# Kernel optimization log

Hardware: AMD Instinct MI355X
Metric: run time of the kernel (lower is better)

Reference implementation:

```python
import jax, jax.numpy as jnp
import numpy as np

# init_kwargs (closed over, matching BaseDepthVolumeModel.__init__)
DEPTH_START = 0.5
DEPTH_END = 10.0
DEPTH_NUM = 64

N_SAMPLES, N_VIEWS, HEIGHT, WIDTH = 2, 4, 256, 320


def _make_extrinsics(key, shape):
    """Random small-rotation-about-y + translation world->camera 4x4 matrices."""
    ang = jax.random.uniform(key, shape, minval=-0.2, maxval=0.2)
    c, s = jnp.cos(ang), jnp.sin(ang)
    z, o = jnp.zeros_like(ang), jnp.ones_like(ang)
    R = jnp.stack([c, z, s, z, o, z, -s, z, c], axis=-1).reshape(*shape, 3, 3)
    t = jax.random.uniform(jax.random.fold_in(key, 1), (*shape, 3), minval=-0.5, maxval=0.5)
    E = jnp.zeros((*shape, 4, 4), jnp.float32)
    E = E.at[..., :3, :3].set(R).at[..., :3, 3].set(t).at[..., 3, 3].set(1.0)
    return E.astype(jnp.float32)


def setup_inputs() -> dict:
    key = jax.random.key(0)
    k1, k2 = jax.random.split(key)
    fx = fy = 200.0
    K = jnp.array([[fx, 0.0, WIDTH / 2.0], [0.0, fy, HEIGHT / 2.0], [0.0, 0.0, 1.0]], jnp.float32)
    return {
        "dst_intrinsics": jnp.broadcast_to(K, (N_SAMPLES, 1, 3, 3)),
        "dst_extrinsics": _make_extrinsics(k1, (N_SAMPLES, 1)),
        "src_intrinsics": jnp.broadcast_to(K, (N_SAMPLES, N_VIEWS, 3, 3)),
        "src_extrinsics": _make_extrinsics(k2, (N_SAMPLES, N_VIEWS)),
        "n_samples": N_SAMPLES,
        "n_views": N_VIEWS,
        "height": HEIGHT,
        "width": WIDTH,
    }


def reference(dst_intrinsics, dst_extrinsics, src_intrinsics, src_extrinsics,
              n_samples, n_views, height, width):
    # Plane-sweep target->source projection for every (sample, view, depth, pixel),
    # fully batched instead of the original triple Python loop.
    depths = jnp.linspace(DEPTH_START, DEPTH_END, DEPTH_NUM).astype(jnp.float32)  # [D]

    Kd = dst_intrinsics[:, 0]                       # [N,3,3]
    Ed = dst_extrinsics[:, 0]                       # [N,4,4]
    # relative transform source_cam <- target_cam:  T = E_src @ inv(E_dst)
    T = jnp.einsum('nvij,njk->nvik', src_extrinsics, jnp.linalg.inv(Ed))  # [N,V,4,4]
    R, t = T[..., :3, :3], T[..., :3, 3]
    A = jnp.einsum('nvij,nvjk->nvik', src_intrinsics, R)                  # K_src @ R  [N,V,3,3]
    b = jnp.einsum('nvij,nvj->nvi', src_intrinsics, t)                    # K_src @ t  [N,V,3]

    # homogeneous pixel grid of the target view, [H,W,3]
    xs = jnp.arange(width, dtype=jnp.float32)
    ys = jnp.arange(height, dtype=jnp.float32)
    X, Y = jnp.meshgrid(xs, ys, indexing='xy')
    grid_h = jnp.stack([X, Y, jnp.ones_like(X)], axis=-1)                 # [H,W,3]

    rays = jnp.einsum('nij,hwj->nhwi', jnp.linalg.inv(Kd), grid_h)        # K_dst^-1 p  [N,H,W,3]
    base = jnp.einsum('nvij,nhwj->nvhwi', A, rays)                        # [N,V,H,W,3]
    # proj = d * (K_src R K_dst^-1 p) + K_src t  -> [N,V,D,H,W,3]
    proj = depths[None, None, :, None, None, None] * base[:, :, None] + b[:, :, None, None, None, :]

    z = proj[..., 2:3]
    z_safe = jnp.where(jnp.abs(z) < 1e-8, 1e-8, z)
    xy = proj[..., :2] / z_safe                                           # source pixel coords

    in_x = (xy[..., 0:1] >= 0.0) & (xy[..., 0:1] <= width - 1)
    in_y = (xy[..., 1:2] >= 0.0) & (xy[..., 1:2] <= height - 1)
    mask = (in_x & in_y & (z > 0.0)).astype(jnp.float32)                  # [N,V,D,H,W,1]

    return xy, mask
```

## Files before the change

kernel.cpp:

```cpp
#include <hip/hip_runtime.h>
#include <math.h>

#define N_S 2
#define N_V 4
#define DQ  64
#define HH  256
#define WW  320
#define WW2 (WW / 2)
#define DPT 16
#define NDC (DQ / DPT)

typedef float f32x4 __attribute__((ext_vector_type(4)));
typedef float f32x2 __attribute__((ext_vector_type(2)));

__global__ __launch_bounds__(256) void fused_warp_kernel(
    const float* __restrict__ Kd,
    const float* __restrict__ Ed,
    const float* __restrict__ Ks,
    const float* __restrict__ Es,
    float* __restrict__ out)
{
    const int HW = HH * WW;
    int idx = blockIdx.x * 256 + threadIdx.x;

    int w2 = idx % WW2;
    int tt = idx / WW2;
    int h  = tt % HH;
    tt /= HH;
    int dc = tt % NDC;
    int nv = tt / NDC;
    int n  = nv >> 2;

    const float* E = Ed + n * 16;
    float Ri[3][3], ti[3];
    #pragma unroll
    for (int r = 0; r < 3; ++r)
        #pragma unroll
        for (int c = 0; c < 3; ++c)
            Ri[r][c] = E[c * 4 + r];
    #pragma unroll
    for (int r = 0; r < 3; ++r)
        ti[r] = -(Ri[r][0] * E[3] + Ri[r][1] * E[7] + Ri[r][2] * E[11]);

    const float* S = Es + nv * 16;
    float Tr[3][3], Tt[3];
    #pragma unroll
    for (int r = 0; r < 3; ++r) {
        #pragma unroll
        for (int c = 0; c < 3; ++c)
            Tr[r][c] = S[r*4+0]*Ri[0][c] + S[r*4+1]*Ri[1][c] + S[r*4+2]*Ri[2][c];
        Tt[r] = S[r*4+0]*ti[0] + S[r*4+1]*ti[1] + S[r*4+2]*ti[2] + S[r*4+3];
    }

    const float* Kv = Ks + nv * 9;
    float A00,A01,A02,A10,A11,A12,A20,A21,A22,b0,b1,b2;
    {
        float Am[3][3], bm[3];
        #pragma unroll
        for (int r = 0; r < 3; ++r) {
            #pragma unroll
            for (int c = 0; c < 3; ++c)
                Am[r][c] = Kv[r*3+0]*Tr[0][c] + Kv[r*3+1]*Tr[1][c] + Kv[r*3+2]*Tr[2][c];
            bm[r] = Kv[r*3+0]*Tt[0] + Kv[r*3+1]*Tt[1] + Kv[r*3+2]*Tt[2];
        }
        A00=Am[0][0];A01=Am[0][1];A02=Am[0][2];
        A10=Am[1][0];A11=Am[1][1];A12=Am[1][2];
        A20=Am[2][0];A21=Am[2][1];A22=Am[2][2];
        b0=bm[0];b1=bm[1];b2=bm[2];
    }

    float ik0,ik1,ik2,ik3,ik4,ik5,ik6,ik7,ik8;
    {
        const float* Km = Kd + n * 9;
        float a=Km[0],b=Km[1],c=Km[2],d=Km[3],e=Km[4],f=Km[5],g=Km[6],hh=Km[7],k=Km[8];
        float det = a*(e*k - f*hh) - b*(d*k - f*g) + c*(d*hh - e*g);
        float inv = 1.0f / det;
        ik0 =  (e*k - f*hh) * inv;
        ik1 = -(b*k - c*hh) * inv;
        ik2 =  (b*f - c*e) * inv;
        ik3 = -(d*k - f*g) * inv;
        ik4 =  (a*k - c*g) * inv;
        ik5 = -(a*f - c*d) * inv;
        ik6 =  (d*hh - e*g) * inv;
        ik7 = -(a*hh - b*g) * inv;
        ik8 =  (a*e - b*d) * inv;
    }

    float X0 = (float)(2 * w2), X1 = X0 + 1.0f, Y = (float)h;

    float rx0 = ik0*X0 + ik1*Y + ik2;
    float ry0 = ik3*X0 + ik4*Y + ik5;
    float rz0 = ik6*X0 + ik7*Y + ik8;
    float rx1 = ik0*X1 + ik1*Y + ik2;
    float ry1 = ik3*X1 + ik4*Y + ik5;
    float rz1 = ik6*X1 + ik7*Y + ik8;

    float bx0 = A00*rx0 + A01*ry0 + A02*rz0;
    float by0 = A10*rx0 + A11*ry0 + A12*rz0;
    float bz0 = A20*rx0 + A21*ry0 + A22*rz0;
    float bx1 = A00*rx1 + A01*ry1 + A02*rz1;
    float by1 = A10*rx1 + A11*ry1 + A12*rz1;
    float bz1 = A20*rx1 + A21*ry1 + A22*rz1;

    size_t pixbase = ((size_t)nv * DQ + (size_t)dc * DPT) * HW
                   + (size_t)h * WW + (size_t)(2 * w2);
    float* __restrict__ mout = out + (size_t)N_S * N_V * DQ * HW * 2;

    const float step = (float)(9.5 / 63.0);
    int d0 = dc * DPT;

    #pragma unroll
    for (int j = 0; j < DPT; ++j) {
        float depth = 0.5f + (float)(d0 + j) * step;

        float px0 = depth*bx0 + b0, py0 = depth*by0 + b1, pz0 = depth*bz0 + b2;
        float px1 = depth*bx1 + b0, py1 = depth*by1 + b1, pz1 = depth*bz1 + b2;

        float zs0 = (fabsf(pz0) < 1e-8f) ? 1e-8f : pz0;
        float zs1 = (fabsf(pz1) < 1e-8f) ? 1e-8f : pz1;

        float x0 = px0 / zs0, y0 = py0 / zs0;
        float x1 = px1 / zs1, y1 = py1 / zs1;

        float m0 = (x0 >= 0.0f && x0 <= (float)(WW-1) &&
                    y0 >= 0.0f && y0 <= (float)(HH-1) && pz0 > 0.0f) ? 1.0f : 0.0f;
        float m1 = (x1 >= 0.0f && x1 <= (float)(WW-1) &&
                    y1 >= 0.0f && y1 <= (float)(HH-1) && pz1 > 0.0f) ? 1.0f : 0.0f;

        size_t p = pixbase + (size_t)j * HW;

        f32x4 xyv; xyv.x = x0; xyv.y = y0; xyv.z = x1; xyv.w = y1;
        __builtin_nontemporal_store(xyv, (f32x4*)(out + 2 * p));
        f32x2 mv; mv.x = m0; mv.y = m1;
        __builtin_nontemporal_store(mv, (f32x2*)(mout + p));
    }
}

extern "C" void kernel_launch(void* const* d_in, const int* in_sizes, int n_in,
                              void* d_out, int out_size, void* d_ws, size_t ws_size,
                              hipStream_t stream) {
    const float* Kd = (const float*)d_in[0];
    const float* Ed = (const float*)d_in[1];
    const float* Ks = (const float*)d_in[2];
    const float* Es = (const float*)d_in[3];

    const long long total = (long long)N_S * N_V * NDC * HH * WW2;
    int blocks = (int)((total + 255) / 256);
    hipLaunchKernelGGL(fused_warp_kernel, dim3(blocks), dim3(256), 0, stream,
                       Kd, Ed, Ks, Es, (float*)d_out);
}
```

Before: 94.95 us.

## Process four pixels per thread with wider stores and reciprocal-based division

Each thread now handles four adjacent pixels and eight depths instead of two pixels and sixteen depths. The mask can then be written with one 16-byte store and the coordinates with two, and an approximate hardware reciprocal with one Newton step replaces the two IEEE divisions per pixel. Launch bounds gain a minimum-occupancy hint. The reciprocal can differ from exact division in the last bits, which may flip mask values right at the image borders.

```diff
diff --git a/kernel.cpp b/kernel.cpp
--- a/kernel.cpp
+++ b/kernel.cpp
@@ -6,14 +6,14 @@
 #define DQ  64
 #define HH  256
 #define WW  320
-#define WW2 (WW / 2)
-#define DPT 16
+#define PX  4
+#define WW4 (WW / PX)
+#define DPT 8
 #define NDC (DQ / DPT)
 
 typedef float f32x4 __attribute__((ext_vector_type(4)));
-typedef float f32x2 __attribute__((ext_vector_type(2)));
 
-__global__ __launch_bounds__(256) void fused_warp_kernel(
+__global__ __launch_bounds__(256, 4) void fused_warp_kernel(
     const float* __restrict__ Kd,
     const float* __restrict__ Ed,
     const float* __restrict__ Ks,
@@ -23,8 +23,8 @@
     const int HW = HH * WW;
     int idx = blockIdx.x * 256 + threadIdx.x;
 
-    int w2 = idx % WW2;
-    int tt = idx / WW2;
+    int w4 = idx % WW4;
+    int tt = idx / WW4;
     int h  = tt % HH;
     tt /= HH;
     int dc = tt % NDC;
@@ -86,24 +86,21 @@
         ik8 =  (a*e - b*d) * inv;
     }
 
-    float X0 = (float)(2 * w2), X1 = X0 + 1.0f, Y = (float)h;
-
-    float rx0 = ik0*X0 + ik1*Y + ik2;
-    float ry0 = ik3*X0 + ik4*Y + ik5;
-    float rz0 = ik6*X0 + ik7*Y + ik8;
-    float rx1 = ik0*X1 + ik1*Y + ik2;
-    float ry1 = ik3*X1 + ik4*Y + ik5;
-    float rz1 = ik6*X1 + ik7*Y + ik8;
-
-    float bx0 = A00*rx0 + A01*ry0 + A02*rz0;
-    float by0 = A10*rx0 + A11*ry0 + A12*rz0;
-    float bz0 = A20*rx0 + A21*ry0 + A22*rz0;
-    float bx1 = A00*rx1 + A01*ry1 + A02*rz1;
-    float by1 = A10*rx1 + A11*ry1 + A12*rz1;
-    float bz1 = A20*rx1 + A21*ry1 + A22*rz1;
+    float Y = (float)h;
+    float bx[PX], by[PX], bz[PX];
+    #pragma unroll
+    for (int p = 0; p < PX; ++p) {
+        float X = (float)(PX * w4 + p);
+        float rx = ik0*X + ik1*Y + ik2;
+        float ry = ik3*X + ik4*Y + ik5;
+        float rz = ik6*X + ik7*Y + ik8;
+        bx[p] = A00*rx + A01*ry + A02*rz;
+        by[p] = A10*rx + A11*ry + A12*rz;
+        bz[p] = A20*rx + A21*ry + A22*rz;
+    }
 
     size_t pixbase = ((size_t)nv * DQ + (size_t)dc * DPT) * HW
-                   + (size_t)h * WW + (size_t)(2 * w2);
+                   + (size_t)h * WW + (size_t)(PX * w4);
     float* __restrict__ mout = out + (size_t)N_S * N_V * DQ * HW * 2;
 
     const float step = (float)(9.5 / 63.0);
@@ -113,26 +110,31 @@
     for (int j = 0; j < DPT; ++j) {
         float depth = 0.5f + (float)(d0 + j) * step;
 
-        float px0 = depth*bx0 + b0, py0 = depth*by0 + b1, pz0 = depth*bz0 + b2;
-        float px1 = depth*bx1 + b0, py1 = depth*by1 + b1, pz1 = depth*bz1 + b2;
+        float x[PX], y[PX], m[PX];
+        #pragma unroll
+        for (int p = 0; p < PX; ++p) {
+            float px = depth*bx[p] + b0;
+            float py = depth*by[p] + b1;
+            float pz = depth*bz[p] + b2;
+            float zs = (fabsf(pz) < 1e-8f) ? 1e-8f : pz;
+            float r  = __builtin_amdgcn_rcpf(zs);
+            r = r * (2.0f - zs * r);
+            x[p] = px * r;
+            y[p] = py * r;
+            m[p] = (x[p] >= 0.0f && x[p] <= (float)(WW-1) &&
+                    y[p] >= 0.0f && y[p] <= (float)(HH-1) &&
+                    pz > 0.0f) ? 1.0f : 0.0f;
+        }
 
-        float zs0 = (fabsf(pz0) < 1e-8f) ? 1e-8f : pz0;
-        float zs1 = (fabsf(pz1) < 1e-8f) ? 1e-8f : pz1;
+        size_t pp = pixbase + (size_t)j * HW;
 
-        float x0 = px0 / zs0, y0 = py0 / zs0;
-        float x1 = px1 / zs1, y1 = py1 / zs1;
+        f32x4 xy0; xy0.x = x[0]; xy0.y = y[0]; xy0.z = x[1]; xy0.w = y[1];
+        f32x4 xy1; xy1.x = x[2]; xy1.y = y[2]; xy1.z = x[3]; xy1.w = y[3];
+        f32x4 mv;  mv.x  = m[0]; mv.y  = m[1]; mv.z  = m[2]; mv.w  = m[3];
 
-        float m0 = (x0 >= 0.0f && x0 <= (float)(WW-1) &&
-                    y0 >= 0.0f && y0 <= (float)(HH-1) && pz0 > 0.0f) ? 1.0f : 0.0f;
-        float m1 = (x1 >= 0.0f && x1 <= (float)(WW-1) &&
-                    y1 >= 0.0f && y1 <= (float)(HH-1) && pz1 > 0.0f) ? 1.0f : 0.0f;
-
-        size_t p = pixbase + (size_t)j * HW;
-
-        f32x4 xyv; xyv.x = x0; xyv.y = y0; xyv.z = x1; xyv.w = y1;
-        __builtin_nontemporal_store(xyv, (f32x4*)(out + 2 * p));
-        f32x2 mv; mv.x = m0; mv.y = m1;
-        __builtin_nontemporal_store(mv, (f32x2*)(mout + p));
+        __builtin_nontemporal_store(xy0, (f32x4*)(out + 2 * pp));
+        __builtin_nontemporal_store(xy1, (f32x4*)(out + 2 * pp + 4));
+        __builtin_nontemporal_store(mv,  (f32x4*)(mout + pp));
     }
 }
 
@@ -144,7 +146,7 @@
     const float* Ks = (const float*)d_in[2];
     const float* Es = (const float*)d_in[3];
 
-    const long long total = (long long)N_S * N_V * NDC * HH * WW2;
+    const long long total = (long long)N_S * N_V * NDC * HH * WW4;
     int blocks = (int)((total + 255) / 256);
     hipLaunchKernelGGL(fused_warp_kernel, dim3(blocks), dim3(256), 0, stream,
                        Kd, Ed, Ks, Es, (float*)d_out);
```

Result: slower. 208.2 us (+119.3%).

## Restructure into per-depth-slice blocks with folded projection matrix and fast reciprocal

Applied to the files above, without the earlier changes.

Each block now handles one (view, depth) slice chunk and folds depth, K_src·R and K_dst^-1 into a single 3x3 affine map, so each pixel needs only a few FMAs. Blocks loop over contiguous pixels, so consecutive iterations write contiguous addresses within one slice instead of striding across depth planes. The per-pixel division is replaced by a hardware reciprocal plus one Newton step. This cuts per-pixel arithmetic but changes rounding relative to the reference's multiply-then-divide order, and it adds integer division by the width inside the loop.

```diff
diff --git a/kernel.cpp b/kernel.cpp
--- a/kernel.cpp
+++ b/kernel.cpp
@@ -6,30 +6,26 @@
 #define DQ  64
 #define HH  256
 #define WW  320
-#define WW2 (WW / 2)
-#define DPT 16
-#define NDC (DQ / DPT)
+#define HW  (HH * WW)
+#define SPLIT 8
+#define CHUNK_PX (HW / SPLIT)
+#define ITERS (CHUNK_PX / (256 * 2))
 
 typedef float f32x4 __attribute__((ext_vector_type(4)));
 typedef float f32x2 __attribute__((ext_vector_type(2)));
 
-__global__ __launch_bounds__(256) void fused_warp_kernel(
+__global__ __launch_bounds__(256) void slice_kernel(
     const float* __restrict__ Kd,
     const float* __restrict__ Ed,
     const float* __restrict__ Ks,
     const float* __restrict__ Es,
     float* __restrict__ out)
 {
-    const int HW = HH * WW;
-    int idx = blockIdx.x * 256 + threadIdx.x;
-
-    int w2 = idx % WW2;
-    int tt = idx / WW2;
-    int h  = tt % HH;
-    tt /= HH;
-    int dc = tt % NDC;
-    int nv = tt / NDC;
-    int n  = nv >> 2;
+    int bid   = blockIdx.x;
+    int chunk = bid % SPLIT;
+    int d     = (bid / SPLIT) % DQ;
+    int nv    = bid / (SPLIT * DQ);
+    int n     = nv >> 2;
 
     const float* E = Ed + n * 16;
     float Ri[3][3], ti[3];
@@ -53,86 +49,88 @@
     }
 
     const float* Kv = Ks + nv * 9;
-    float A00,A01,A02,A10,A11,A12,A20,A21,A22,b0,b1,b2;
-    {
-        float Am[3][3], bm[3];
+    float Am[3][3], bm[3];
+    #pragma unroll
+    for (int r = 0; r < 3; ++r) {
         #pragma unroll
-        for (int r = 0; r < 3; ++r) {
-            #pragma unroll
-            for (int c = 0; c < 3; ++c)
-                Am[r][c] = Kv[r*3+0]*Tr[0][c] + Kv[r*3+1]*Tr[1][c] + Kv[r*3+2]*Tr[2][c];
-            bm[r] = Kv[r*3+0]*Tt[0] + Kv[r*3+1]*Tt[1] + Kv[r*3+2]*Tt[2];
-        }
-        A00=Am[0][0];A01=Am[0][1];A02=Am[0][2];
-        A10=Am[1][0];A11=Am[1][1];A12=Am[1][2];
-        A20=Am[2][0];A21=Am[2][1];A22=Am[2][2];
-        b0=bm[0];b1=bm[1];b2=bm[2];
+        for (int c = 0; c < 3; ++c)
+            Am[r][c] = Kv[r*3+0]*Tr[0][c] + Kv[r*3+1]*Tr[1][c] + Kv[r*3+2]*Tr[2][c];
+        bm[r] = Kv[r*3+0]*Tt[0] + Kv[r*3+1]*Tt[1] + Kv[r*3+2]*Tt[2];
     }
 
-    float ik0,ik1,ik2,ik3,ik4,ik5,ik6,ik7,ik8;
+    float IK[3][3];
     {
         const float* Km = Kd + n * 9;
-        float a=Km[0],b=Km[1],c=Km[2],d=Km[3],e=Km[4],f=Km[5],g=Km[6],hh=Km[7],k=Km[8];
-        float det = a*(e*k - f*hh) - b*(d*k - f*g) + c*(d*hh - e*g);
+        float a=Km[0],b=Km[1],c=Km[2],dd=Km[3],e=Km[4],f=Km[5],g=Km[6],hh=Km[7],k=Km[8];
+        float det = a*(e*k - f*hh) - b*(dd*k - f*g) + c*(dd*hh - e*g);
         float inv = 1.0f / det;
-        ik0 =  (e*k - f*hh) * inv;
-        ik1 = -(b*k - c*hh) * inv;
-        ik2 =  (b*f - c*e) * inv;
-        ik3 = -(d*k - f*g) * inv;
-        ik4 =  (a*k - c*g) * inv;
-        ik5 = -(a*f - c*d) * inv;
-        ik6 =  (d*hh - e*g) * inv;
-        ik7 = -(a*hh - b*g) * inv;
-        ik8 =  (a*e - b*d) * inv;
+        IK[0][0] =  (e*k - f*hh) * inv;
+        IK[0][1] = -(b*k - c*hh) * inv;
+        IK[0][2] =  (b*f - c*e) * inv;
+        IK[1][0] = -(dd*k - f*g) * inv;
+        IK[1][1] =  (a*k - c*g) * inv;
+        IK[1][2] = -(a*f - c*dd) * inv;
+        IK[2][0] =  (dd*hh - e*g) * inv;
+        IK[2][1] = -(a*hh - b*g) * inv;
+        IK[2][2] =  (a*e - b*dd) * inv;
     }
 
-    float X0 = (float)(2 * w2), X1 = X0 + 1.0f, Y = (float)h;
+    const float step = (float)(9.5 / 63.0);
+    float depth = 0.5f + (float)d * step;
+    float Q[3][3], cvec[3];
+    #pragma unroll
+    for (int r = 0; r < 3; ++r) {
+        #pragma unroll
+        for (int c = 0; c < 3; ++c)
+            Q[r][c] = depth * (Am[r][0]*IK[0][c] + Am[r][1]*IK[1][c] + Am[r][2]*IK[2][c]);
+        cvec[r] = Q[r][2] + bm[r];
+    }
+    float Q00=Q[0][0], Q01=Q[0][1], c0=cvec[0];
+    float Q10=Q[1][0], Q11=Q[1][1], c1=cvec[1];
+    float Q20=Q[2][0], Q21=Q[2][1], c2=cvec[2];
 
-    float rx0 = ik0*X0 + ik1*Y + ik2;
-    float ry0 = ik3*X0 + ik4*Y + ik5;
-    float rz0 = ik6*X0 + ik7*Y + ik8;
-    float rx1 = ik0*X1 + ik1*Y + ik2;
-    float ry1 = ik3*X1 + ik4*Y + ik5;
-    float rz1 = ik6*X1 + ik7*Y + ik8;
+    size_t slice = (size_t)nv * DQ + (size_t)d;
+    float* __restrict__ xyp = out + slice * (size_t)HW * 2 + (size_t)chunk * CHUNK_PX * 2;
+    float* __restrict__ mp  = out + (size_t)N_S * N_V * DQ * HW * 2
+                            + slice * (size_t)HW + (size_t)chunk * CHUNK_PX;
 
-    float bx0 = A00*rx0 + A01*ry0 + A02*rz0;
-    float by0 = A10*rx0 + A11*ry0 + A12*rz0;
-    float bz0 = A20*rx0 + A21*ry0 + A22*rz0;
-    float bx1 = A00*rx1 + A01*ry1 + A02*rz1;
-    float by1 = A10*rx1 + A11*ry1 + A12*rz1;
-    float bz1 = A20*rx1 + A21*ry1 + A22*rz1;
+    int t2 = threadIdx.x * 2;
+    int gbase = chunk * CHUNK_PX + t2;
 
-    size_t pixbase = ((size_t)nv * DQ + (size_t)dc * DPT) * HW
-                   + (size_t)h * WW + (size_t)(2 * w2);
-    float* __restrict__ mout = out + (size_t)N_S * N_V * DQ * HW * 2;
+    #pragma unroll 4
+    for (int j = 0; j < ITERS; ++j) {
+        int pix  = j * 512 + t2;
+        int gpix = gbase + j * 512;
+        int h = gpix / WW;
+        int w = gpix - h * WW;
+        float X = (float)w, Y = (float)h;
 
-    const float step = (float)(9.5 / 63.0);
-    int d0 = dc * DPT;
-
-    #pragma unroll
-    for (int j = 0; j < DPT; ++j) {
-        float depth = 0.5f + (float)(d0 + j) * step;
-
-        float px0 = depth*bx0 + b0, py0 = depth*by0 + b1, pz0 = depth*bz0 + b2;
-        float px1 = depth*bx1 + b0, py1 = depth*by1 + b1, pz1 = depth*bz1 + b2;
+        float px0 = Q00*X + Q01*Y + c0;
+        float py0 = Q10*X + Q11*Y + c1;
+        float pz0 = Q20*X + Q21*Y + c2;
+        float px1 = px0 + Q00;
+        float py1 = py0 + Q10;
+        float pz1 = pz0 + Q20;
 
         float zs0 = (fabsf(pz0) < 1e-8f) ? 1e-8f : pz0;
         float zs1 = (fabsf(pz1) < 1e-8f) ? 1e-8f : pz1;
+        float r0 = __builtin_amdgcn_rcpf(zs0);
+        r0 = r0 * (2.0f - zs0 * r0);
+        float r1 = __builtin_amdgcn_rcpf(zs1);
+        r1 = r1 * (2.0f - zs1 * r1);
 
-        float x0 = px0 / zs0, y0 = py0 / zs0;
-        float x1 = px1 / zs1, y1 = py1 / zs1;
+        float x0 = px0 * r0, y0 = py0 * r0;
+        float x1 = px1 * r1, y1 = py1 * r1;
 
         float m0 = (x0 >= 0.0f && x0 <= (float)(WW-1) &&
                     y0 >= 0.0f && y0 <= (float)(HH-1) && pz0 > 0.0f) ? 1.0f : 0.0f;
         float m1 = (x1 >= 0.0f && x1 <= (float)(WW-1) &&
                     y1 >= 0.0f && y1 <= (float)(HH-1) && pz1 > 0.0f) ? 1.0f : 0.0f;
 
-        size_t p = pixbase + (size_t)j * HW;
-
         f32x4 xyv; xyv.x = x0; xyv.y = y0; xyv.z = x1; xyv.w = y1;
-        __builtin_nontemporal_store(xyv, (f32x4*)(out + 2 * p));
+        __builtin_nontemporal_store(xyv, (f32x4*)(xyp + (size_t)pix * 2));
         f32x2 mv; mv.x = m0; mv.y = m1;
-        __builtin_nontemporal_store(mv, (f32x2*)(mout + p));
+        __builtin_nontemporal_store(mv, (f32x2*)(mp + pix));
     }
 }
 
@@ -144,8 +142,7 @@
     const float* Ks = (const float*)d_in[2];
     const float* Es = (const float*)d_in[3];
 
-    const long long total = (long long)N_S * N_V * NDC * HH * WW2;
-    int blocks = (int)((total + 255) / 256);
-    hipLaunchKernelGGL(fused_warp_kernel, dim3(blocks), dim3(256), 0, stream,
+    int blocks = N_S * N_V * DQ * SPLIT;
+    hipLaunchKernelGGL(slice_kernel, dim3(blocks), dim3(256), 0, stream,
                        Kd, Ed, Ks, Es, (float*)d_out);
 }
```

New measurement: 102.1 us. +7.5%, slower.

## Split fused kernel into separate xy and mask kernels with rcp division

Applied to the files above, without the earlier changes.

Splits the single fused kernel into two launches. One writes only the xy coordinates, two pixels per thread as 16-byte stores. The other recomputes the projection for four pixels per thread so the mask can also be written with 16-byte stores instead of 8-byte ones. Division is replaced by a hardware reciprocal plus one Newton step. The cost is an extra launch, duplicated projection arithmetic in the mask kernel, and results that may differ slightly from IEEE division near the mask boundaries.

```diff
diff --git a/kernel.cpp b/kernel.cpp
--- a/kernel.cpp
+++ b/kernel.cpp
@@ -6,23 +6,70 @@
 #define DQ  64
 #define HH  256
 #define WW  320
-#define WW2 (WW / 2)
+#define HW  (HH * WW)
 #define DPT 16
 #define NDC (DQ / DPT)
+#define WW2 (WW / 2)
+#define WW4 (WW / 4)
 
 typedef float f32x4 __attribute__((ext_vector_type(4)));
-typedef float f32x2 __attribute__((ext_vector_type(2)));
-
-__global__ __launch_bounds__(256) void fused_warp_kernel(
-    const float* __restrict__ Kd,
-    const float* __restrict__ Ed,
-    const float* __restrict__ Ks,
-    const float* __restrict__ Es,
+
+__device__ __forceinline__ void camera_setup(
+    const float* __restrict__ Kd, const float* __restrict__ Ed,
+    const float* __restrict__ Ks, const float* __restrict__ Es,
+    int nv, int n, float Am[3][3], float bm[3], float IK[3][3])
+{
+    const float* E = Ed + n * 16;
+    float Ri[3][3], ti[3];
+    #pragma unroll
+    for (int r = 0; r < 3; ++r)
+        #pragma unroll
+        for (int c = 0; c < 3; ++c)
+            Ri[r][c] = E[c * 4 + r];
+    #pragma unroll
+    for (int r = 0; r < 3; ++r)
+        ti[r] = -(Ri[r][0] * E[3] + Ri[r][1] * E[7] + Ri[r][2] * E[11]);
+
+    const float* S = Es + nv * 16;
+    float Tr[3][3], Tt[3];
+    #pragma unroll
+    for (int r = 0; r < 3; ++r) {
+        #pragma unroll
+        for (int c = 0; c < 3; ++c)
+            Tr[r][c] = S[r*4+0]*Ri[0][c] + S[r*4+1]*Ri[1][c] + S[r*4+2]*Ri[2][c];
+        Tt[r] = S[r*4+0]*ti[0] + S[r*4+1]*ti[1] + S[r*4+2]*ti[2] + S[r*4+3];
+    }
+
+    const float* Kv = Ks + nv * 9;
+    #pragma unroll
+    for (int r = 0; r < 3; ++r) {
+        #pragma unroll
+        for (int c = 0; c < 3; ++c)
+            Am[r][c] = Kv[r*3+0]*Tr[0][c] + Kv[r*3+1]*Tr[1][c] + Kv[r*3+2]*Tr[2][c];
+        bm[r] = Kv[r*3+0]*Tt[0] + Kv[r*3+1]*Tt[1] + Kv[r*3+2]*Tt[2];
+    }
+
+    const float* Km = Kd + n * 9;
+    float a=Km[0],b=Km[1],c=Km[2],dd=Km[3],e=Km[4],f=Km[5],g=Km[6],hh=Km[7],k=Km[8];
+    float det = a*(e*k - f*hh) - b*(dd*k - f*g) + c*(dd*hh - e*g);
+    float inv = 1.0f / det;
+    IK[0][0] =  (e*k - f*hh) * inv;
+    IK[0][1] = -(b*k - c*hh) * inv;
+    IK[0][2] =  (b*f - c*e) * inv;
+    IK[1][0] = -(dd*k - f*g) * inv;
+    IK[1][1] =  (a*k - c*g) * inv;
+    IK[1][2] = -(a*f - c*dd) * inv;
+    IK[2][0] =  (dd*hh - e*g) * inv;
+    IK[2][1] = -(a*hh - b*g) * inv;
+    IK[2][2] =  (a*e - b*dd) * inv;
+}
+
+__global__ __launch_bounds__(256) void xy_kernel(
+    const float* __restrict__ Kd, const float* __restrict__ Ed,
+    const float* __restrict__ Ks, const float* __restrict__ Es,
     float* __restrict__ out)
 {
-    const int HW = HH * WW;
     int idx = blockIdx.x * 256 + threadIdx.x;
-
     int w2 = idx % WW2;
     int tt = idx / WW2;
     int h  = tt % HH;
@@ -31,80 +78,27 @@
     int nv = tt / NDC;
     int n  = nv >> 2;
 
-    const float* E = Ed + n * 16;
-    float Ri[3][3], ti[3];
-    #pragma unroll
-    for (int r = 0; r < 3; ++r)
-        #pragma unroll
-        for (int c = 0; c < 3; ++c)
-            Ri[r][c] = E[c * 4 + r];
-    #pragma unroll
-    for (int r = 0; r < 3; ++r)
-        ti[r] = -(Ri[r][0] * E[3] + Ri[r][1] * E[7] + Ri[r][2] * E[11]);
-
-    const float* S = Es + nv * 16;
-    float Tr[3][3], Tt[3];
-    #pragma unroll
-    for (int r = 0; r < 3; ++r) {
-        #pragma unroll
-        for (int c = 0; c < 3; ++c)
-            Tr[r][c] = S[r*4+0]*Ri[0][c] + S[r*4+1]*Ri[1][c] + S[r*4+2]*Ri[2][c];
-        Tt[r] = S[r*4+0]*ti[0] + S[r*4+1]*ti[1] + S[r*4+2]*ti[2] + S[r*4+3];
-    }
-
-    const float* Kv = Ks + nv * 9;
-    float A00,A01,A02,A10,A11,A12,A20,A21,A22,b0,b1,b2;
-    {
-        float Am[3][3], bm[3];
-        #pragma unroll
-        for (int r = 0; r < 3; ++r) {
-            #pragma unroll
-            for (int c = 0; c < 3; ++c)
-                Am[r][c] = Kv[r*3+0]*Tr[0][c] + Kv[r*3+1]*Tr[1][c] + Kv[r*3+2]*Tr[2][c];
-            bm[r] = Kv[r*3+0]*Tt[0] + Kv[r*3+1]*Tt[1] + Kv[r*3+2]*Tt[2];
-        }
-        A00=Am[0][0];A01=Am[0][1];A02=Am[0][2];
-        A10=Am[1][0];A11=Am[1][1];A12=Am[1][2];
-        A20=Am[2][0];A21=Am[2][1];A22=Am[2][2];
-        b0=bm[0];b1=bm[1];b2=bm[2];
-    }
-
-    float ik0,ik1,ik2,ik3,ik4,ik5,ik6,ik7,ik8;
-    {
-        const float* Km = Kd + n * 9;
-        float a=Km[0],b=Km[1],c=Km[2],d=Km[3],e=Km[4],f=Km[5],g=Km[6],hh=Km[7],k=Km[8];
-        float det = a*(e*k - f*hh) - b*(d*k - f*g) + c*(d*hh - e*g);
-        float inv = 1.0f / det;
-        ik0 =  (e*k - f*hh) * inv;
-        ik1 = -(b*k - c*hh) * inv;
-        ik2 =  (b*f - c*e) * inv;
-        ik3 = -(d*k - f*g) * inv;
-        ik4 =  (a*k - c*g) * inv;
-        ik5 = -(a*f - c*d) * inv;
-        ik6 =  (d*hh - e*g) * inv;
-        ik7 = -(a*hh - b*g) * inv;
-        ik8 =  (a*e - b*d) * inv;
-    }
+    float Am[3][3], bm[3], IK[3][3];
+    camera_setup(Kd, Ed, Ks, Es, nv, n, Am, bm, IK);
+    float b0 = bm[0], b1 = bm[1], b2 = bm[2];
 
     float X0 = (float)(2 * w2), X1 = X0 + 1.0f, Y = (float)h;
-
-    float rx0 = ik0*X0 + ik1*Y + ik2;
-    float ry0 = ik3*X0 + ik4*Y + ik5;
-    float rz0 = ik6*X0 + ik7*Y + ik8;
-    float rx1 = ik0*X1 + ik1*Y + ik2;
-    float ry1 = ik3*X1 + ik4*Y + ik5;
-    float rz1 = ik6*X1 + ik7*Y + ik8;
-
-    float bx0 = A00*rx0 + A01*ry0 + A02*rz0;
-    float by0 = A10*rx0 + A11*ry0 + A12*rz0;
-    float bz0 = A20*rx0 + A21*ry0 + A22*rz0;
-    float bx1 = A00*rx1 + A01*ry1 + A02*rz1;
-    float by1 = A10*rx1 + A11*ry1 + A12*rz1;
-    float bz1 = A20*rx1 + A21*ry1 + A22*rz1;
+    float rx0 = IK[0][0]*X0 + IK[0][1]*Y + IK[0][2];
+    float ry0 = IK[1][0]*X0 + IK[1][1]*Y + IK[1][2];
+    float rz0 = IK[2][0]*X0 + IK[2][1]*Y + IK[2][2];
+    float rx1 = IK[0][0]*X1 + IK[0][1]*Y + IK[0][2];
+    float ry1 = IK[1][0]*X1 + IK[1][1]*Y + IK[1][2];
+    float rz1 = IK[2][0]*X1 + IK[2][1]*Y + IK[2][2];
+
+    float bx0 = Am[0][0]*rx0 + Am[0][1]*ry0 + Am[0][2]*rz0;
+    float by0 = Am[1][0]*rx0 + Am[1][1]*ry0 + Am[1][2]*rz0;
+    float bz0 = Am[2][0]*rx0 + Am[2][1]*ry0 + Am[2][2]*rz0;
+    float bx1 = Am[0][0]*rx1 + Am[0][1]*ry1 + Am[0][2]*rz1;
+    float by1 = Am[1][0]*rx1 + Am[1][1]*ry1 + Am[1][2]*rz1;
+    float bz1 = Am[2][0]*rx1 + Am[2][1]*ry1 + Am[2][2]*rz1;
 
     size_t pixbase = ((size_t)nv * DQ + (size_t)dc * DPT) * HW
                    + (size_t)h * WW + (size_t)(2 * w2);
-    float* __restrict__ mout = out + (size_t)N_S * N_V * DQ * HW * 2;
 
     const float step = (float)(9.5 / 63.0);
     int d0 = dc * DPT;
@@ -118,21 +112,74 @@
 
         float zs0 = (fabsf(pz0) < 1e-8f) ? 1e-8f : pz0;
         float zs1 = (fabsf(pz1) < 1e-8f) ? 1e-8f : pz1;
-
-        float x0 = px0 / zs0, y0 = py0 / zs0;
-        float x1 = px1 / zs1, y1 = py1 / zs1;
-
-        float m0 = (x0 >= 0.0f && x0 <= (float)(WW-1) &&
-                    y0 >= 0.0f && y0 <= (float)(HH-1) && pz0 > 0.0f) ? 1.0f : 0.0f;
-        float m1 = (x1 >= 0.0f && x1 <= (float)(WW-1) &&
-                    y1 >= 0.0f && y1 <= (float)(HH-1) && pz1 > 0.0f) ? 1.0f : 0.0f;
+        float r0 = __builtin_amdgcn_rcpf(zs0); r0 = r0 * (2.0f - zs0 * r0);
+        float r1 = __builtin_amdgcn_rcpf(zs1); r1 = r1 * (2.0f - zs1 * r1);
+
+        f32x4 xyv;
+        xyv.x = px0 * r0; xyv.y = py0 * r0;
+        xyv.z = px1 * r1; xyv.w = py1 * r1;
 
         size_t p = pixbase + (size_t)j * HW;
-
-        f32x4 xyv; xyv.x = x0; xyv.y = y0; xyv.z = x1; xyv.w = y1;
         __builtin_nontemporal_store(xyv, (f32x4*)(out + 2 * p));
-        f32x2 mv; mv.x = m0; mv.y = m1;
-        __builtin_nontemporal_store(mv, (f32x2*)(mout + p));
+    }
+}
+
+__global__ __launch_bounds__(256) void mask_kernel(
+    const float* __restrict__ Kd, const float* __restrict__ Ed,
+    const float* __restrict__ Ks, const float* __restrict__ Es,
+    float* __restrict__ out)
+{
+    int idx = blockIdx.x * 256 + threadIdx.x;
+    int w4 = idx % WW4;
+    int tt = idx / WW4;
+    int h  = tt % HH;
+    tt /= HH;
+    int dc = tt % NDC;
+    int nv = tt / NDC;
+    int n  = nv >> 2;
+
+    float Am[3][3], bm[3], IK[3][3];
+    camera_setup(Kd, Ed, Ks, Es, nv, n, Am, bm, IK);
+    float b0 = bm[0], b1 = bm[1], b2 = bm[2];
+
+    float Y = (float)h;
+    float bx[4], by[4], bz[4];
+    #pragma unroll
+    for (int p = 0; p < 4; ++p) {
+        float X = (float)(4 * w4 + p);
+        float rx = IK[0][0]*X + IK[0][1]*Y + IK[0][2];
+        float ry = IK[1][0]*X + IK[1][1]*Y + IK[1][2];
+        float rz = IK[2][0]*X + IK[2][1]*Y + IK[2][2];
+        bx[p] = Am[0][0]*rx + Am[0][1]*ry + Am[0][2]*rz;
+        by[p] = Am[1][0]*rx + Am[1][1]*ry + Am[1][2]*rz;
+        bz[p] = Am[2][0]*rx + Am[2][1]*ry + Am[2][2]*rz;
+    }
+
+    float* __restrict__ mout = out + (size_t)N_S * N_V * DQ * HW * 2;
+    size_t pixbase = ((size_t)nv * DQ + (size_t)dc * DPT) * HW
+                   + (size_t)h * WW + (size_t)(4 * w4);
+
+    const float step = (float)(9.5 / 63.0);
+    int d0 = dc * DPT;
+
+    #pragma unroll
+    for (int j = 0; j < DPT; ++j) {
+        float depth = 0.5f + (float)(d0 + j) * step;
+        f32x4 mv;
+        #pragma unroll
+        for (int p = 0; p < 4; ++p) {
+            float px = depth*bx[p] + b0;
+            float py = depth*by[p] + b1;
+            float pz = depth*bz[p] + b2;
+            float zs = (fabsf(pz) < 1e-8f) ? 1e-8f : pz;
+            float r  = __builtin_amdgcn_rcpf(zs); r = r * (2.0f - zs * r);
+            float x = px * r, y = py * r;
+            float m = (x >= 0.0f && x <= (float)(WW-1) &&
+                       y >= 0.0f && y <= (float)(HH-1) && pz > 0.0f) ? 1.0f : 0.0f;
+            mv[p] = m;
+        }
+        size_t p = pixbase + (size_t)j * HW;
+        __builtin_nontemporal_store(mv, (f32x4*)(mout + p));
     }
 }
 
@@ -143,9 +190,13 @@
     const float* Ed = (const float*)d_in[1];
     const float* Ks = (const float*)d_in[2];
     const float* Es = (const float*)d_in[3];
-
-    const long long total = (long long)N_S * N_V * NDC * HH * WW2;
-    int blocks = (int)((total + 255) / 256);
-    hipLaunchKernelGGL(fused_warp_kernel, dim3(blocks), dim3(256), 0, stream,
-                       Kd, Ed, Ks, Es, (float*)d_out);
-}
+    float* out = (float*)d_out;
+
+    int xy_blocks   = (N_S * N_V * NDC * HH * WW2) / 256;
+    int mask_blocks = (N_S * N_V * NDC * HH * WW4) / 256;
+
+    hipLaunchKernelGGL(xy_kernel,   dim3(xy_blocks),   dim3(256), 0, stream,
+                       Kd, Ed, Ks, Es, out);
+    hipLaunchKernelGGL(mask_kernel, dim3(mask_blocks), dim3(256), 0, stream,
+                       Kd, Ed, Ks, Es, out);
+}
```

Result: faster. 91.77 us (-3.3%).
